# Kernel tuning notes

Hardware: AMD Instinct MI355X
Metric: run time of the kernel (lower is better)

Reference implementation:

```python
import jax, jax.numpy as jnp
import numpy as np

DIM = 384; HEADS = 16; HEAD_DIM = DIM // HEADS; HID = 4 * DIM
ETA_SCALE = 0.01; CLIP_INNER = 1.0; EPS = 1e-5
B = 8; T_FR = 32; GH = 16; GW = 16; CHUNK = 8; N = T_FR * GH * GW
D_SEG = 2 * (HEAD_DIM // 3 // 2)  # 8 dims each for t/h/w rotation (3*8 == head_dim)


def _layernorm(x, g, b):
    m = jnp.mean(x, -1, keepdims=True)
    v = jnp.var(x, -1, keepdims=True)
    return (x - m) * jax.lax.rsqrt(v + EPS) * g + b


def _mlp(W1, b1, W2, b2, x):
    # 2-layer Titan memory / CMS level MLP: dim -> 4*dim -> dim, GELU
    return jax.nn.gelu(x @ W1 + b1) @ W2 + b2


def _rope_seg(x, pos):
    # x: [..., s] interleaved-pair RoPE with positions pos (broadcastable to x[..., 0])
    s = x.shape[-1]; half = s // 2
    freqs = 1.0 / (10000.0 ** (jnp.arange(half, dtype=x.dtype) / half))
    ang = pos[..., None] * freqs
    c, si = jnp.cos(ang), jnp.sin(ang)
    x1, x2 = x[..., 0::2], x[..., 1::2]
    return jnp.stack([x1 * c - x2 * si, x1 * si + x2 * c], -1).reshape(x.shape)


def _apply_rope(x, tp, hp, wp):
    # 3D RoPE per head over (t, h, w) position segments
    b, n, d = x.shape
    xh = x.reshape(b, n, HEADS, HEAD_DIM)
    s = D_SEG
    parts = [_rope_seg(xh[..., 0:s], tp[None, :, None]),
             _rope_seg(xh[..., s:2 * s], hp[None, :, None]),
             _rope_seg(xh[..., 2 * s:3 * s], wp[None, :, None])]
    if 3 * s < HEAD_DIM:
        parts.append(xh[..., 3 * s:])
    return jnp.concatenate(parts, -1).reshape(b, n, d)


def _forward(x, norm1_g, norm1_b, q_W, tW1, tb1, tW2, tb2, out_W, out_b,
             norm2_g, norm2_b, cms_W1, cms_b1, cms_W2, cms_b2, T, H, W, chunk_size):
    Bx, Nt, D = x.shape
    y = _layernorm(x, norm1_g, norm1_b)
    nc = T // chunk_size
    Cper = chunk_size * H * W
    y_ch = y.reshape(Bx, nc, Cper, D).swapaxes(0, 1)  # [nc, B, Cper, D]
    # per-chunk RoPE positions (positions restart each chunk, matching _titan_forward_chunk)
    tp = jnp.repeat(jnp.arange(chunk_size, dtype=x.dtype), H * W)
    hp = jnp.tile(jnp.repeat(jnp.arange(H, dtype=x.dtype), W), chunk_size)
    wp = jnp.tile(jnp.arange(W, dtype=x.dtype), chunk_size * H)

    def mem_loss(W1, b1, W2, b2, kk, tt):
        return jnp.mean((_mlp(W1, b1, W2, b2, kk) - tt) ** 2)

    grad_fn = jax.grad(mem_loss, argnums=(0, 1, 2, 3))
    mlp_v = jax.vmap(_mlp, in_axes=(0, 0, 0, 0, None))

    def step(carry, yc):
        W1s, b1s, W2s, b2s = carry  # stacked [5, ...]: k, v, eta, alpha, memory
        gen = mlp_v(W1s[:4], b1s[:4], W2s[:4], b2s[:4], yc)  # [4, B, C, D]
        k, v, eta_raw, alpha_raw = gen[0], gen[1], gen[2], gen[3]
        eta = jax.nn.softplus(eta_raw) * ETA_SCALE
        alpha = jax.nn.sigmoid(alpha_raw)
        q = yc @ q_W
        q = _apply_rope(q, tp, hp, wp)
        k = _apply_rope(k, tp, hp, wp)
        out = _mlp(W1s[4], b1s[4], W2s[4], b2s[4], q)  # retrieve from main memory
        # surprise signal (per-token retrieval error norm); threshold=0 -> always update
        # surprise = jnp.linalg.norm(v - out, axis=-1)
        # self-targets v_hat = M_box(v) for the 4 adaptive memories; main memory targets v
        vhat = mlp_v(W1s[:4], b1s[:4], W2s[:4], b2s[:4], v)
        targets = jnp.concatenate([jax.lax.stop_gradient(vhat), v[None]], 0)  # [5,B,C,D]
        g1, g2, g3, g4 = jax.vmap(grad_fn, in_axes=(0, 0, 0, 0, None, 0))(
            W1s, b1s, W2s, b2s, k, targets)
        norm = jnp.sqrt(jnp.sum(g1 * g1, (1, 2)) + jnp.sum(g2 * g2, 1)
                        + jnp.sum(g3 * g3, (1, 2)) + jnp.sum(g4 * g4, 1))
        sc = jnp.minimum(1.0, CLIP_INNER / (norm + 1e-12))  # inner grad clip per memory
        em = jnp.mean(eta); am = jnp.mean(alpha)
        # DGD update with decay alpha and lr eta: p <- (1-alpha)*p - eta*g
        W1n = (1 - am) * W1s - em * g1 * sc[:, None, None]
        b1n = (1 - am) * b1s - em * g2 * sc[:, None]
        W2n = (1 - am) * W2s - em * g3 * sc[:, None, None]
        b2n = (1 - am) * b2s - em * g4 * sc[:, None]
        return (W1n, b1n, W2n, b2n), out

    _, outs = jax.lax.scan(step, (tW1, tb1, tW2, tb2), y_ch)
    titan = outs.swapaxes(0, 1).reshape(Bx, Nt, D) @ out_W + out_b
    x2 = x + titan
    # Phase B: CMS multi-frequency MLP cascade (sequential chain of level MLPs)
    h = _layernorm(x2, norm2_g, norm2_b)
    for l in range(cms_W1.shape[0]):
        h = _mlp(cms_W1[l], cms_b1[l], cms_W2[l], cms_b2[l], h)
    return x2 + h


def setup_inputs() -> dict:
    key = jax.random.key(0)
    ks = jax.random.split(key, 8)
    s = 0.02
    f = jnp.float32
    return {
        'x': jax.random.normal(ks[0], (B, N, DIM), f),
        'norm1_g': jnp.ones((DIM,), f), 'norm1_b': jnp.zeros((DIM,), f),
        'q_W': jax.random.normal(ks[1], (DIM, DIM), f) * s,
        'tW1': jax.random.normal(ks[2], (5, DIM, HID), f) * s,
        'tb1': jnp.zeros((5, HID), f),
        'tW2': jax.random.normal(ks[3], (5, HID, DIM), f) * s,
        'tb2': jnp.zeros((5, DIM), f),
        'out_W': jax.random.normal(ks[4], (DIM, DIM), f) * s,
        'out_b': jnp.zeros((DIM,), f),
        'norm2_g': jnp.ones((DIM,), f), 'norm2_b': jnp.zeros((DIM,), f),
        'cms_W1': jax.random.normal(ks[5], (3, DIM, HID), f) * s,
        'cms_b1': jnp.zeros((3, HID), f),
        'cms_W2': jax.random.normal(ks[6], (3, HID, DIM), f) * s,
        'cms_b2': jnp.zeros((3, DIM), f),
        'T': T_FR, 'H': GH, 'W': GW, 'chunk_size': CHUNK,
    }


def reference(x, norm1_g, norm1_b, q_W, tW1, tb1, tW2, tb2, out_W, out_b,
              norm2_g, norm2_b, cms_W1, cms_b1, cms_W2, cms_b2, T, H, W, chunk_size):
    return _forward(x, norm1_g, norm1_b, q_W, tW1, tb1, tW2, tb2, out_W, out_b,
                    norm2_g, norm2_b, cms_W1, cms_b1, cms_W2, cms_b2, T, H, W, chunk_size)
```

## Files before the change

### kernel.cpp

```cpp
#include <hip/hip_runtime.h>
#include <cstddef>
#include <cstdint>


typedef __bf16 bf16;
typedef __bf16 bf16x4 __attribute__((ext_vector_type(4)));
typedef __bf16 bf16x8 __attribute__((ext_vector_type(8)));
typedef float  f32x4  __attribute__((ext_vector_type(4)));

constexpr float INV_CNT = 1.0f / 6291456.0f;

__device__ __forceinline__ float fast_gelu(float x) {
  float u = 0.7978845608028654f * (x + 0.044715f * x * x * x);
  return x / (1.0f + __expf(-2.0f * u));
}
__device__ __forceinline__ f32x4 gelu4(f32x4 v) {
  v[0] = fast_gelu(v[0]); v[1] = fast_gelu(v[1]);
  v[2] = fast_gelu(v[2]); v[3] = fast_gelu(v[3]);
  return v;
}
__device__ __forceinline__ void gelu_both4(f32x4 v, f32x4& g, f32x4& gp) {
#pragma unroll
  for (int e = 0; e < 4; ++e) {
    float x = v[e];
    float x2 = x * x;
    float u = 0.7978845608028654f * (x + 0.044715f * x * x2);
    float s = 1.0f / (1.0f + __expf(-2.0f * u));
    g[e]  = x * s;
    gp[e] = s + x * s * (1.0f - s) * 1.5957691216057308f * (1.0f + 0.134145f * x2);
  }
}
__device__ __forceinline__ bf16x4 tobf4(f32x4 v) {
  bf16x4 o; o[0] = (bf16)v[0]; o[1] = (bf16)v[1]; o[2] = (bf16)v[2]; o[3] = (bf16)v[3];
  return o;
}
__device__ __forceinline__ f32x4 tof4(bf16x4 v) {
  return f32x4{(float)v[0], (float)v[1], (float)v[2], (float)v[3]};
}

__device__ __forceinline__ void gload16(const bf16* g, void* lds) {
  __builtin_amdgcn_global_load_lds(
      (const __attribute__((address_space(1))) void*)g,
      (__attribute__((address_space(3))) void*)lds, 16, 0, 0);
}

template <int N>
__device__ __forceinline__ void wait_vmcnt() {
  if constexpr (N == 0)      asm volatile("s_waitcnt vmcnt(0)" ::: "memory");
  else if constexpr (N == 2) asm volatile("s_waitcnt vmcnt(2)" ::: "memory");
  else if constexpr (N == 3) asm volatile("s_waitcnt vmcnt(3)" ::: "memory");
  else if constexpr (N == 4) asm volatile("s_waitcnt vmcnt(4)" ::: "memory");
  __builtin_amdgcn_sched_barrier(0);
}

__device__ __forceinline__ int xcd_chunk(int id, int n) {
  int q = n >> 3, r = n & 7;
  int xcd = id & 7, pos = id >> 3;
  return (xcd < r ? xcd * (q + 1) : r * (q + 1) + (xcd - r) * q) + pos;
}

__global__ __launch_bounds__(64)
void ln_kernel(const float* __restrict__ x, const float* __restrict__ g,
               const float* __restrict__ b, bf16* __restrict__ y,
               int shift, int base, int stride) {
  int r = blockIdx.x;
  int src = ((r >> shift) * stride) + base + (r & ((1 << shift) - 1));
  int lane = threadIdx.x;
  const float* xr = x + (size_t)src * 384;
  float vals[6];
  float s = 0.f, s2 = 0.f;
#pragma unroll
  for (int i = 0; i < 6; ++i) {
    float v = xr[lane + i * 64];
    vals[i] = v; s += v; s2 += v * v;
  }
#pragma unroll
  for (int o = 32; o > 0; o >>= 1) { s += __shfl_xor(s, o); s2 += __shfl_xor(s2, o); }
  float m = s * (1.0f / 384.0f);
  float var = s2 * (1.0f / 384.0f) - m * m;
  float rr = rsqrtf(var + 1e-5f);
  bf16* yr = y + (size_t)r * 384;
#pragma unroll
  for (int i = 0; i < 6; ++i) {
    int c = lane + i * 64;
    yr[c] = (bf16)((vals[i] - m) * rr * g[c] + b[c]);
  }
}

__device__ __forceinline__ void trw_body(const float* in, bf16* out, int R, int C,
                                         int c0, int r0, int tid) {
  __shared__ float t[32][33];
  int tr = tid >> 3, tc = (tid & 7) * 4;
  f32x4 v = *(const f32x4*)&in[(size_t)(r0 + tr) * C + c0 + tc];
  t[tr][tc + 0] = v[0]; t[tr][tc + 1] = v[1]; t[tr][tc + 2] = v[2]; t[tr][tc + 3] = v[3];
  __syncthreads();
  bf16x4 o;
  o[0] = (bf16)t[tc + 0][tr]; o[1] = (bf16)t[tc + 1][tr];
  o[2] = (bf16)t[tc + 2][tr]; o[3] = (bf16)t[tc + 3][tr];
  *(bf16x4*)&out[(size_t)(c0 + tr) * R + r0 + tc] = o;
}

__global__ __launch_bounds__(256)
void trans_state(const float* __restrict__ SW1, const float* __restrict__ SW2,
                 bf16* __restrict__ sw1t, bf16* __restrict__ sw2t) {
  int z = blockIdx.z;
  if (z < 5)
    trw_body(SW1 + (size_t)z * 589824, sw1t + (size_t)z * 589824, 384, 1536,
             blockIdx.x * 32, blockIdx.y * 32, threadIdx.x);
  else
    trw_body(SW2 + (size_t)(z - 5) * 589824, sw2t + (size_t)(z - 5) * 589824, 1536, 384,
             blockIdx.y * 32, blockIdx.x * 32, threadIdx.x);
}

__global__ __launch_bounds__(256)
void trans_static(const float* __restrict__ qW, const float* __restrict__ outW,
                  const float* __restrict__ cW1, const float* __restrict__ cW2,
                  bf16* __restrict__ qwt, bf16* __restrict__ owt,
                  bf16* __restrict__ cw1t, bf16* __restrict__ cw2t) {
  int z = blockIdx.z;
  if (z < 2) {
    if (blockIdx.x >= 12) return;
    trw_body(z ? outW : qW, z ? owt : qwt, 384, 384,
             blockIdx.x * 32, blockIdx.y * 32, threadIdx.x);
  } else if (z < 5) {
    int lc = z - 2;
    trw_body(cW1 + (size_t)lc * 589824, cw1t + (size_t)lc * 589824, 384, 1536,
             blockIdx.x * 32, blockIdx.y * 32, threadIdx.x);
  } else {
    int lc = z - 5;
    trw_body(cW2 + (size_t)lc * 589824, cw2t + (size_t)lc * 589824, 1536, 384,
             blockIdx.y * 32, blockIdx.x * 32, threadIdx.x);
  }
}

__global__ __launch_bounds__(256)
void tr_bf(const bf16* __restrict__ in, bf16* __restrict__ out, int R, int C) {
  __shared__ bf16 t[32][36];
  int r0 = blockIdx.x * 32, c0 = blockIdx.y * 32;
  int tr = threadIdx.x >> 3, tc = (threadIdx.x & 7) * 4;
  bf16x4 v = *(const bf16x4*)&in[(size_t)(r0 + tr) * C + c0 + tc];
  t[tr][tc + 0] = v[0]; t[tr][tc + 1] = v[1]; t[tr][tc + 2] = v[2]; t[tr][tc + 3] = v[3];
  __syncthreads();
  bf16x4 o;
  o[0] = t[tc + 0][tr]; o[1] = t[tc + 1][tr]; o[2] = t[tc + 2][tr]; o[3] = t[tc + 3][tr];
  *(bf16x4*)&out[(size_t)(c0 + tr) * R + r0 + tc] = o;
}

__global__ __launch_bounds__(256)
void copy_bf16(const float* __restrict__ in, bf16* __restrict__ out, int n) {
  int i = (blockIdx.x * 256 + threadIdx.x) * 4;
  if (i < n) {
    f32x4 v = *(const f32x4*)&in[i];
    *(bf16x4*)&out[i] = tobf4(v);
  }
}

enum { E_BF16 = 0, E_GELU, E_PAIR, E_PAIRD, E_SUB, E_SCL, E_MUL, E_F32ADD, E_KV, E_RED2 };

template <int EPI, int BM>
__global__ __launch_bounds__(BM == 128 ? 512 : 256)
void mm_fwd(const bf16* __restrict__ Act, int lda, const bf16* __restrict__ W,
            const float* __restrict__ bias, const bf16* __restrict__ baux,
            const float* __restrict__ faux, float* __restrict__ red,
            bf16* __restrict__ Cb, bf16* __restrict__ C2, bf16* __restrict__ Ct,
            float* __restrict__ Cf, int K, int ldc, int ldt, float scale,
            int croff, int cshift, int cbase, int cstride,
            long zA, long zW, int zB) {
  constexpr int NW = (BM == 128) ? 8 : 4;
  constexpr int NFM = 2;
  constexpr int TW = 8 / NW;
  constexpr int TA = (BM / 16) / NW;
  constexpr int LPT = TW + TA;
  constexpr int SWE = 128 * 32;
  constexpr int SAE = BM * 32;
  constexpr int BUFE = 2 * (SWE + SAE);
  constexpr int SLABE = NW * 16 * 68 * 2;
  constexpr int SMEME = (BUFE > SLABE) ? BUFE : SLABE;
  constexpr bool TRANS = (EPI == E_PAIR || EPI == E_PAIRD || EPI == E_SUB ||
                          EPI == E_SCL || EPI == E_MUL);
  __shared__ bf16 smem[SMEME];
  const int z = blockIdx.z;
  Act += (size_t)z * zA;
  W   += (size_t)z * zW;
  if (bias) bias += (size_t)z * zB;
  const int nx = gridDim.x;
  const int nid = xcd_chunk(blockIdx.y * nx + blockIdx.x, nx * gridDim.y);
  const int m0 = (nid / nx) * BM, i0 = (nid % nx) * 128;
  const int tid = threadIdx.x;
  const int l = tid & 63, w = tid >> 6;
  const int a = l & 15, g = l >> 4;
  const int wi0 = (w & 1) * 64, wm0 = (w >> 1) * 32;
  const int srow = l >> 2;
  const int sue = ((l & 3) ^ ((l >> 3) & 3)) * 8;
  const int fru = (g ^ ((a >> 1) & 3)) << 4;

  const bf16* wp = W   + (size_t)(i0 + srow) * K   + sue;
  const bf16* ap = Act + (size_t)(m0 + srow) * lda + sue;

  f32x4 acc[4][NFM];
#pragma unroll
  for (int i = 0; i < 4; ++i)
#pragma unroll
    for (int j = 0; j < NFM; ++j) acc[i][j] = f32x4{0.f, 0.f, 0.f, 0.f};

  auto stage = [&](int buf, int k0) {
    bf16* dW = smem + buf * SWE;
    bf16* dA = smem + 2 * SWE + buf * SAE;
#pragma unroll
    for (int t = 0; t < TW; ++t) {
      const int seg = w * TW + t;
      gload16(wp + (size_t)(seg * 16) * K + k0, (char*)dW + seg * 1024);
    }
#pragma unroll
    for (int t = 0; t < TA; ++t) {
      const int seg = w * TA + t;
      gload16(ap + (size_t)(seg * 16) * lda + k0, (char*)dA + seg * 1024);
    }
  };

  const int nIt = K >> 5;
  stage(0, 0);
  for (int it = 0; it < nIt; ++it) {
    const int cur = it & 1;
    if (it + 1 < nIt) { stage(cur ^ 1, (it + 1) << 5); wait_vmcnt<LPT>(); }
    else              { wait_vmcnt<0>(); }
    __builtin_amdgcn_s_barrier();
    const bf16* bW = smem + cur * SWE;
    const bf16* bA = smem + 2 * SWE + cur * SAE;
    {
      bf16x8 Af[4], Bf[NFM];
#pragma unroll
      for (int f = 0; f < 4; ++f) {
        const int rW = wi0 + f * 16 + a;
        Af[f] = *(const bf16x8*)((const char*)bW + rW * 64 + fru);
      }
#pragma unroll
      for (int f = 0; f < NFM; ++f) {
        const int rA = wm0 + f * 16 + a;
        Bf[f] = *(const bf16x8*)((const char*)bA + rA * 64 + fru);
      }
#pragma unroll
      for (int fi = 0; fi < 4; ++fi)
#pragma unroll
        for (int fm = 0; fm < NFM; ++fm)
          acc[fi][fm] = __builtin_amdgcn_mfma_f32_16x16x32_bf16(Af[fi], Bf[fm], acc[fi][fm], 0, 0, 0);
    }
    asm volatile("s_waitcnt lgkmcnt(0)" ::: "memory");
    __builtin_amdgcn_s_barrier();
  }

  if constexpr (EPI == E_RED2) {
    float ssum = 0.f;
#pragma unroll
    for (int fi = 0; fi < 4; ++fi) {
      f32x4 b4 = *(const f32x4*)&bias[i0 + wi0 + fi * 16 + g * 4];
#pragma unroll
      for (int fm = 0; fm < NFM; ++fm)
#pragma unroll
        for (int r = 0; r < 4; ++r) {
          float vv = acc[fi][fm][r] + b4[r];
          if (z == 0) ssum += fmaxf(vv, 0.f) + log1pf(__expf(-fabsf(vv)));
          else        ssum += 1.0f / (1.0f + __expf(-vv));
        }
    }
#pragma unroll
    for (int o = 32; o > 0; o >>= 1) ssum += __shfl_xor(ssum, o);
    float* wred = (float*)smem;
    if (l == 0) wred[w] = ssum;
    __syncthreads();
    if (tid == 0) {
      float t2 = 0.f;
      for (int q = 0; q < NW; ++q) t2 += wred[q];
      atomicAdd(&red[z], t2);
    }
    return;
  } else {
    float* T = (float*)smem + w * (16 * 68);
    const int iB = i0 + wi0;
    f32x4 b4 = f32x4{0.f, 0.f, 0.f, 0.f};
    if (bias) b4 = *(const f32x4*)&bias[iB + a * 4];
#pragma unroll
    for (int fm = 0; fm < NFM; ++fm) {
#pragma unroll
      for (int fi = 0; fi < 4; ++fi)
        *(f32x4*)&T[a * 68 + fi * 16 + g * 4] = acc[fi][fm];
      asm volatile("s_waitcnt lgkmcnt(0)" ::: "memory");
      __builtin_amdgcn_sched_barrier(0);

#pragma unroll
      for (int q = 0; q < 4; ++q) {
        const int ml = wm0 + fm * 16 + q * 4 + g;
        const int trow = q * 4 + g;
        f32x4 v = *(const f32x4*)&T[trow * 68 + a * 4];
        v += b4;
        if constexpr (EPI == E_F32ADD) {
          const int rr = croff + m0 + ml;
          const int crow = ((rr >> cshift) * cstride) + cbase + (rr & ((1 << cshift) - 1));
          const size_t cb = (size_t)crow * ldc + iB + a * 4;
          v += *(const f32x4*)&faux[cb];
          *(f32x4*)&Cf[cb] = v;
        } else {
          const size_t cb = (size_t)(m0 + ml) * ldc + iB + a * 4;
          if constexpr (EPI == E_BF16) {
            *(bf16x4*)&Cb[cb] = tobf4(v);
          } else if constexpr (EPI == E_KV) {
            bf16* DST = (z == 0) ? Cb : C2;
            *(bf16x4*)&DST[cb] = tobf4(v);
          } else if constexpr (EPI == E_GELU) {
            *(bf16x4*)&Cb[cb] = tobf4(gelu4(v));
          } else if constexpr (EPI == E_PAIR) {
            f32x4 gv, gp;
            gelu_both4(v, gv, gp);
            *(bf16x4*)&Cb[cb] = tobf4(gp);
            *(bf16x4*)&C2[cb] = tobf4(gv);
            *(f32x4*)&T[trow * 68 + a * 4] = gv;
          } else if constexpr (EPI == E_PAIRD) {
            f32x4 gv, gp;
            gelu_both4(v, gv, gp);
            f32x4 d = gv - tof4(*(const bf16x4*)&baux[cb]);
            *(bf16x4*)&Cb[cb] = tobf4(gp);
            *(bf16x4*)&C2[cb] = tobf4(d);
            *(f32x4*)&T[trow * 68 + a * 4] = gv;
          } else if constexpr (EPI == E_SUB) {
            f32x4 t4 = tof4(*(const bf16x4*)&baux[cb]);
            v = (v - t4) * scale;
            *(bf16x4*)&Cb[cb] = tobf4(v);
            *(f32x4*)&T[trow * 68 + a * 4] = v;
          } else if constexpr (EPI == E_SCL) {
            v = v * scale;
            *(bf16x4*)&Cb[cb] = tobf4(v);
            *(f32x4*)&T[trow * 68 + a * 4] = v;
          } else if constexpr (EPI == E_MUL) {
            f32x4 h4 = tof4(*(const bf16x4*)&baux[cb]);
            v *= h4;
            *(f32x4*)&T[trow * 68 + a * 4] = v;
          }
        }
      }

      if constexpr (TRANS) {
        asm volatile("s_waitcnt lgkmcnt(0)" ::: "memory");
        __builtin_amdgcn_sched_barrier(0);
        const int mg = m0 + wm0 + fm * 16;
        bf16x8 o0, o1;
#pragma unroll
        for (int j = 0; j < 16; ++j) {
          float vv = T[j * 68 + l];
          if (j < 8) o0[j] = (bf16)vv; else o1[j - 8] = (bf16)vv;
        }
        *(bf16x8*)&Ct[(size_t)(iB + l) * ldt + mg] = o0;
        *(bf16x8*)&Ct[(size_t)(iB + l) * ldt + mg + 8] = o1;
      }
    }
  }
}

__global__ __launch_bounds__(512)
void mm_tn2c(const bf16* __restrict__ P1, int ldP1, const bf16* __restrict__ Q1, int ldQ1,
             float* __restrict__ Ga, int ldGa,
             const bf16* __restrict__ P2, int ldP2, const bf16* __restrict__ Q2, int ldQ2,
             float* __restrict__ Gb, int ldGb, int mlen,
             float* __restrict__ G4s, float* __restrict__ G2s) {
  constexpr int SBE = 128 * 32;
  __shared__ bf16 smem[4 * SBE];
  const int nid = xcd_chunk(blockIdx.x, gridDim.x);
  const int grp = nid / 36, pair = nid % 36;
  const int part = grp & 1, zsl = grp >> 1;
  const bf16* P; const bf16* Q; float* G; float* Gsum;
  int ldP, ldQ, ldG, p0, q0;
  if (part == 0) {
    P = P1; Q = Q1; G = Ga; ldP = ldP1; ldQ = ldQ1; ldG = ldGa; Gsum = G4s;
    p0 = (pair / 3) * 128; q0 = (pair % 3) * 128;
  } else {
    P = P2; Q = Q2; G = Gb; ldP = ldP2; ldQ = ldQ2; ldG = ldGb; Gsum = G2s;
    p0 = (pair / 12) * 128; q0 = (pair % 12) * 128;
  }
  const bool doSum = (p0 == 0);
  const int tid = threadIdx.x;
  const int mb = zsl * mlen;
  const int l = tid & 63, w = tid >> 6;
  const int a = l & 15, g = l >> 4;
  const int wp0 = (w & 1) * 64, wq0 = (w >> 1) * 32;
  const int sue = ((l & 3) ^ ((l >> 3) & 3)) * 8;
  const int fru = (g ^ ((a >> 1) & 3)) << 4;

  const bf16* pP = P + (size_t)(p0 + w * 16 + (l >> 2)) * ldP + sue;
  const bf16* pQ = Q + (size_t)(q0 + w * 16 + (l >> 2)) * ldQ + sue;

  f32x4 acc[4][2];
#pragma unroll
  for (int i = 0; i < 4; ++i)
#pragma unroll
    for (int j = 0; j < 2; ++j) acc[i][j] = f32x4{0.f, 0.f, 0.f, 0.f};
  float qsum = 0.f;
  const int sumoff = (w * 16 + (l >> 2)) * 64 + (l & 3) * 16;

  auto stage = [&](int buf, int m0) {
    bf16* dP = smem + buf * SBE;
    bf16* dQ = smem + 2 * SBE + buf * SBE;
    gload16(pP + m0, (char*)dP + w * 1024);
    gload16(pQ + m0, (char*)dQ + w * 1024);
  };

  const int nIt = mlen >> 5;
  stage(0, mb);
  for (int it = 0; it < nIt; ++it) {
    const int cur = it & 1;
    if (it + 1 < nIt) { stage(cur ^ 1, mb + ((it + 1) << 5)); wait_vmcnt<2>(); }
    else              { wait_vmcnt<0>(); }
    __builtin_amdgcn_s_barrier();
    const bf16* bP = smem + cur * SBE;
    const bf16* bQ = smem + 2 * SBE + cur * SBE;
    {
      bf16x8 Pf[4], Qf[2];
#pragma unroll
      for (int f = 0; f < 4; ++f) {
        const int rP = wp0 + f * 16 + a;
        Pf[f] = *(const bf16x8*)((const char*)bP + rP * 64 + fru);
      }
#pragma unroll
      for (int f = 0; f < 2; ++f) {
        const int rQ = wq0 + f * 16 + a;
        Qf[f] = *(const bf16x8*)((const char*)bQ + rQ * 64 + fru);
      }
#pragma unroll
      for (int f1 = 0; f1 < 4; ++f1)
#pragma unroll
        for (int f2 = 0; f2 < 2; ++f2)
          acc[f1][f2] = __builtin_amdgcn_mfma_f32_16x16x32_bf16(Pf[f1], Qf[f2], acc[f1][f2], 0, 0, 0);
    }
    if (doSum) {
      bf16x8 s0 = *(const bf16x8*)((const char*)bQ + sumoff);
#pragma unroll
      for (int e = 0; e < 8; ++e) qsum += (float)s0[e];
    }
    asm volatile("s_waitcnt lgkmcnt(0)" ::: "memory");
    __builtin_amdgcn_s_barrier();
  }
#pragma unroll
  for (int f1 = 0; f1 < 4; ++f1)
#pragma unroll
    for (int f2 = 0; f2 < 2; ++f2)
#pragma unroll
      for (int r = 0; r < 4; ++r)
        atomicAdd(&G[(size_t)(p0 + wp0 + f1 * 16 + g * 4 + r) * ldG + q0 + wq0 + f2 * 16 + a],
                  acc[f1][f2][r]);
  if (doSum) {
    qsum += __shfl_xor(qsum, 1);
    qsum += __shfl_xor(qsum, 2);
    if ((l & 3) == 0) atomicAdd(&Gsum[q0 + w * 16 + (l >> 2)], qsum);
  }
}

__global__ __launch_bounds__(256)
void rope_kernel(bf16* __restrict__ qb, int rbase) {
  int idx = blockIdx.x * blockDim.x + threadIdx.x;
  int row = idx >> 4, hd = idx & 15;
  int j = (rbase + row) & 2047;
  float pos[3] = { (float)(j >> 8), (float)((j >> 4) & 15), (float)(j & 15) };
  const float freqs[4] = { 1.0f, 0.1f, 0.01f, 0.001f };
  bf16* p = qb + (size_t)row * 384 + hd * 24;
#pragma unroll
  for (int s = 0; s < 3; ++s) {
    bf16x8 vv = *(bf16x8*)(p + s * 8);
#pragma unroll
    for (int pr = 0; pr < 4; ++pr) {
      float ang = pos[s] * freqs[pr];
      float si, co;
      sincosf(ang, &si, &co);
      float e0 = (float)vv[2 * pr], e1 = (float)vv[2 * pr + 1];
      vv[2 * pr]     = (bf16)(e0 * co - e1 * si);
      vv[2 * pr + 1] = (bf16)(e0 * si + e1 * co);
    }
    *(bf16x8*)(p + s * 8) = vv;
  }
}

__global__ __launch_bounds__(256)
void sumsq_all(const float* __restrict__ G1, const float* __restrict__ G2,
               const float* __restrict__ G3, const float* __restrict__ G4,
               float* __restrict__ red) {
  int i = blockIdx.y, bx = blockIdx.x;
  const float* base; int per, lb, nb;
  if (bx < 256)      { base = G1 + (size_t)i * 589824; per = 589824; lb = bx;       nb = 256; }
  else if (bx < 512) { base = G3 + (size_t)i * 589824; per = 589824; lb = bx - 256; nb = 256; }
  else if (bx < 514) { base = G2 + (size_t)i * 1536;   per = 1536;   lb = bx - 512; nb = 2; }
  else               { base = G4 + (size_t)i * 384;    per = 384;    lb = bx - 514; nb = 2; }
  float s = 0.f;
  for (int idx = lb * 256 + threadIdx.x; idx < per; idx += nb * 256) {
    float v = base[idx]; s += v * v;
  }
  __shared__ float sm[256];
  sm[threadIdx.x] = s; __syncthreads();
  for (int o = 128; o > 0; o >>= 1) {
    if (threadIdx.x < o) sm[threadIdx.x] += sm[threadIdx.x + o];
    __syncthreads();
  }
  if (threadIdx.x == 0) atomicAdd(&red[2 + i], sm[0]);
}

__global__ __launch_bounds__(256)
void update_all(float* __restrict__ SW1, float* __restrict__ SB1,
                float* __restrict__ SW2, float* __restrict__ SB2,
                const float* __restrict__ G1, const float* __restrict__ G2,
                const float* __restrict__ G3, const float* __restrict__ G4,
                const float* __restrict__ red) {
  int i = blockIdx.y, bx = blockIdx.x;
  float* S; const float* G; int per, lb, nb;
  if (bx < 512)       { S = SW1; G = G1; per = 589824; lb = bx;        nb = 512; }
  else if (bx < 1024) { S = SW2; G = G3; per = 589824; lb = bx - 512;  nb = 512; }
  else if (bx < 1028) { S = SB1; G = G2; per = 1536;   lb = bx - 1024; nb = 4; }
  else                { S = SB2; G = G4; per = 384;    lb = bx - 1028; nb = 4; }
  size_t base = (size_t)i * per;
  float em = 0.01f * red[0] * INV_CNT;
  float am = red[1] * INV_CNT;
  float norm = sqrtf(red[2 + i]);
  float sc = fminf(1.0f, 1.0f / (norm + 1e-12f));
  float ws_ = 1.0f - am;
  float gs = em * sc;
  for (int idx = lb * 256 + (int)threadIdx.x; idx < per; idx += nb * 256)
    S[base + idx] = ws_ * S[base + idx] - gs * G[base + idx];
}

extern "C" void kernel_launch(void* const* d_in, const int* in_sizes, int n_in,
                              void* d_out, int out_size, void* d_ws, size_t ws_size,
                              hipStream_t stream) {
  const float* x    = (const float*)d_in[0];
  const float* n1g  = (const float*)d_in[1];
  const float* n1b  = (const float*)d_in[2];
  const float* qW   = (const float*)d_in[3];
  const float* tW1  = (const float*)d_in[4];
  const float* tb1  = (const float*)d_in[5];
  const float* tW2  = (const float*)d_in[6];
  const float* tb2  = (const float*)d_in[7];
  const float* outW = (const float*)d_in[8];
  const float* outb = (const float*)d_in[9];
  const float* n2g  = (const float*)d_in[10];
  const float* n2b  = (const float*)d_in[11];
  const float* cW1  = (const float*)d_in[12];
  const float* cb1  = (const float*)d_in[13];
  const float* cW2  = (const float*)d_in[14];
  const float* cb2  = (const float*)d_in[15];
  float* out = (float*)d_out;

  const size_t W1SZ = 384 * 1536, W2SZ = 1536 * 384;
  const size_t STATE = 5 * W1SZ + 5 * 1536 + 5 * W2SZ + 5 * 384;
  const size_t BF_W = 21 * W1SZ + 2 * 147456;
  const size_t CHUNK_BF = 4 * (size_t)16384 * 384;
  const size_t FIXEDF = 2 * STATE + 16 + BF_W / 2 + CHUNK_BF / 2;
  size_t MS = 16384;
  while (MS > 2048 && (FIXEDF + MS * 3840) * 4 > ws_size) MS >>= 1;
  if ((FIXEDF + MS * 3840) * 4 > ws_size) {
    hipMemcpyAsync(d_out, d_in[0], (size_t)25165824 * 4, hipMemcpyDeviceToDevice, stream);
    return;
  }
  const int NS = (int)(16384 / MS);
  const int iMS = (int)MS;

  float* ws = (float*)d_ws;
  size_t off = 0;
  auto alloc = [&](size_t n) { float* p = ws + off; off += n; return p; };
  auto balloc = [&](size_t n) { bf16* p = (bf16*)(ws + off); off += (n + 1) / 2; return p; };
  float* SW1 = alloc(5 * W1SZ);
  float* SB1 = alloc(5 * 1536);
  float* SW2 = alloc(5 * W2SZ);
  float* SB2 = alloc(5 * 384);
  float* G1  = alloc(5 * W1SZ);
  float* G2  = alloc(5 * 1536);
  float* G3  = alloc(5 * W2SZ);
  float* G4  = alloc(5 * 384);
  float* RED = alloc(16);
  bf16* Yc   = balloc((size_t)16384 * 384);
  bf16* Kb   = balloc((size_t)16384 * 384);
  bf16* Vb   = balloc((size_t)16384 * 384);
  bf16* Kbt  = balloc((size_t)16384 * 384);
  bf16* sw1t = balloc(5 * W1SZ);
  bf16* sw2t = balloc(5 * W2SZ);
  bf16* sw2c = balloc(5 * W2SZ);
  bf16* qwt  = balloc(147456);
  bf16* owt  = balloc(147456);
  bf16* cw1t = balloc(3 * W1SZ);
  bf16* cw2t = balloc(3 * W2SZ);
  bf16* pool = balloc(MS * 3072);
  bf16* GH1t = balloc(MS * 1536);
  bf16* DAt  = balloc(MS * 1536);
  bf16* OD   = balloc(MS * 384);
  bf16* ODt  = balloc(MS * 384);
  bf16* T2   = balloc(MS * 384);
  bf16* Tt   = balloc(MS * 384);
  bf16* H1r  = pool;
  bf16* GH1k = pool + MS * 1536;

  hipMemcpyAsync(SW1, tW1, 5 * W1SZ * 4, hipMemcpyDeviceToDevice, stream);
  hipMemcpyAsync(SB1, tb1, 5 * 1536 * 4, hipMemcpyDeviceToDevice, stream);
  hipMemcpyAsync(SW2, tW2, 5 * W2SZ * 4, hipMemcpyDeviceToDevice, stream);
  hipMemcpyAsync(SB2, tb2, 5 * 384 * 4, hipMemcpyDeviceToDevice, stream);

  trans_static<<<dim3(48, 12, 8), 256, 0, stream>>>(qW, outW, cW1, cW2, qwt, owt, cw1t, cw2t);

  const size_t grads_bytes = STATE * 4;
  const int gm  = iMS / 128;
  const int gm2 = iMS / 64;
  int mlen_t = iMS / 8; if (mlen_t < 128) mlen_t = 128;
  if (mlen_t > 2048) mlen_t = 2048;
  const int nzt = iMS / mlen_t;
  const int tn_grid = 36 * 2 * nzt;
  const float SC = 2.0f * INV_CNT;
  const size_t MSR = (size_t)iMS * 384;

  for (int c = 0; c < 4; ++c) {
    hipMemsetAsync(G1, 0, grads_bytes, stream);
    hipMemsetAsync(RED, 0, 64, stream);
    trans_state<<<dim3(48, 12, 10), 256, 0, stream>>>(SW1, SW2, sw1t, sw2t);
    copy_bf16<<<dim3(2880), 256, 0, stream>>>(SW2, sw2c, (int)(5 * W2SZ));

    ln_kernel<<<dim3(16384), dim3(64), 0, stream>>>(x, n1g, n1b, Yc, 11, c * 2048, 8192);

    for (int s = 0; s < NS; ++s) {
      const bf16* Ys = Yc + (size_t)s * MSR;
      mm_fwd<E_GELU, 128><<<dim3(24, gm), 512, 0, stream>>>(Ys, 384, sw1t,
          SB1, nullptr, nullptr, nullptr, pool, nullptr, nullptr, nullptr,
          384, 3072, 0, 0.f, 0, 30, 0, 0, 0, 0, 0);
      mm_fwd<E_KV, 64><<<dim3(3, gm2, 2), 256, 0, stream>>>(pool, 3072, sw2t,
          SB2, nullptr, nullptr, nullptr, Kb + s * MSR, Vb + s * MSR, nullptr, nullptr,
          1536, 384, 0, 0.f, 0, 30, 0, 0, 1536, (long)W2SZ, 384);
      mm_fwd<E_GELU, 128><<<dim3(24, gm), 512, 0, stream>>>(Ys, 384, sw1t + 2 * W1SZ,
          SB1 + 2 * 1536, nullptr, nullptr, nullptr, pool, nullptr, nullptr, nullptr,
          384, 3072, 0, 0.f, 0, 30, 0, 0, 0, 0, 0);
      mm_fwd<E_RED2, 64><<<dim3(3, gm2, 2), 256, 0, stream>>>(pool, 3072, sw2t + 2 * W2SZ,
          SB2 + 2 * 384, nullptr, nullptr, RED, nullptr, nullptr, nullptr, nullptr,
          1536, 384, 0, 0.f, 0, 30, 0, 0, 1536, (long)W2SZ, 384);
    }

    for (int s = 0; s < NS; ++s) {
      const bf16* Ys = Yc + (size_t)s * MSR;
      mm_fwd<E_BF16, 64><<<dim3(3, gm2), 256, 0, stream>>>(Ys, 384, qwt,
          nullptr, nullptr, nullptr, nullptr, Tt, nullptr, nullptr, nullptr,
          384, 384, 0, 0.f, 0, 30, 0, 0, 0, 0, 0);
      rope_kernel<<<dim3(iMS / 16), 256, 0, stream>>>(Tt, s * iMS);
      mm_fwd<E_GELU, 128><<<dim3(12, gm), 512, 0, stream>>>(Tt, 384, sw1t + 4 * W1SZ,
          SB1 + 4 * 1536, nullptr, nullptr, nullptr, GH1k, nullptr, nullptr, nullptr,
          384, 1536, 0, 0.f, 0, 30, 0, 0, 0, 0, 0);
      mm_fwd<E_BF16, 64><<<dim3(3, gm2), 256, 0, stream>>>(GH1k, 1536, sw2t + 4 * W2SZ,
          SB2 + 4 * 384, nullptr, nullptr, nullptr, T2, nullptr, nullptr, nullptr,
          1536, 384, 0, 0.f, 0, 30, 0, 0, 0, 0, 0);
      mm_fwd<E_F32ADD, 64><<<dim3(3, gm2), 256, 0, stream>>>(T2, 384, owt, outb,
          nullptr, x, nullptr, nullptr, nullptr, nullptr, out,
          384, 384, 0, 0.f, s * iMS, 11, c * 2048, 8192, 0, 0, 0);
    }

    rope_kernel<<<dim3(1024), 256, 0, stream>>>(Kb, 0);
    tr_bf<<<dim3(512, 12), 256, 0, stream>>>(Kb, Kbt, 16384, 384);

    for (int s = 0; s < NS; ++s) {
      const bf16* Ks = Kb + (size_t)s * MSR;
      const bf16* Vs = Vb + (size_t)s * MSR;
      for (int i = 0; i < 5; ++i) {
        if (i < 4) {
          mm_fwd<E_GELU, 128><<<dim3(12, gm), 512, 0, stream>>>(Vs, 384, sw1t + i * W1SZ,
              SB1 + i * 1536, nullptr, nullptr, nullptr, GH1k, nullptr, nullptr, nullptr,
              384, 1536, 0, 0.f, 0, 30, 0, 0, 0, 0, 0);
          mm_fwd<E_PAIRD, 128><<<dim3(12, gm), 512, 0, stream>>>(Ks, 384, sw1t + i * W1SZ,
              SB1 + i * 1536, GH1k, nullptr, nullptr, H1r, DAt, GH1t, nullptr,
              384, 1536, iMS, 0.f, 0, 30, 0, 0, 0, 0, 0);
          mm_fwd<E_SCL, 64><<<dim3(3, gm2), 256, 0, stream>>>(DAt, 1536, sw2t + i * W2SZ,
              nullptr, nullptr, nullptr, nullptr, OD, nullptr, ODt, nullptr,
              1536, 384, iMS, SC, 0, 30, 0, 0, 0, 0, 0);
        } else {
          mm_fwd<E_PAIR, 128><<<dim3(12, gm), 512, 0, stream>>>(Ks, 384, sw1t + 4 * W1SZ,
              SB1 + 4 * 1536, nullptr, nullptr, nullptr, H1r, GH1k, GH1t, nullptr,
              384, 1536, iMS, 0.f, 0, 30, 0, 0, 0, 0, 0);
          mm_fwd<E_SUB, 64><<<dim3(3, gm2), 256, 0, stream>>>(GH1k, 1536, sw2t + 4 * W2SZ,
              SB2 + 4 * 384, Vs, nullptr, nullptr, OD, nullptr, ODt, nullptr,
              1536, 384, iMS, SC, 0, 30, 0, 0, 0, 0, 0);
        }
        mm_fwd<E_MUL, 128><<<dim3(12, gm), 512, 0, stream>>>(OD, 384, sw2c + i * W2SZ,
            nullptr, H1r, nullptr, nullptr, nullptr, nullptr, DAt, nullptr,
            384, 1536, iMS, 0.f, 0, 30, 0, 0, 0, 0, 0);
        mm_tn2c<<<dim3(tn_grid), 512, 0, stream>>>(
            GH1t, iMS, ODt, iMS, G3 + i * W2SZ, 384,
            Kbt + (size_t)s * iMS, 16384, DAt, iMS, G1 + i * W1SZ, 1536, mlen_t,
            G4 + i * 384, G2 + i * 1536);
      }
    }

    sumsq_all<<<dim3(516, 5), 256, 0, stream>>>(G1, G2, G3, G4, RED);
    update_all<<<dim3(1032, 5), 256, 0, stream>>>(SW1, SB1, SW2, SB2, G1, G2, G3, G4, RED);
  }

  const int NCS = (int)(65536 / MS);
  for (int s2 = 0; s2 < NCS; ++s2) {
    float* outp = out + (size_t)s2 * MSR;
    ln_kernel<<<dim3(iMS), dim3(64), 0, stream>>>(out, n2g, n2b, OD, 30, s2 * iMS, 0);
    bf16* hc = OD; bf16* hn = T2;
    for (int lc = 0; lc < 3; ++lc) {
      mm_fwd<E_GELU, 128><<<dim3(12, gm), 512, 0, stream>>>(hc, 384, cw1t + lc * W1SZ,
          cb1 + lc * 1536, nullptr, nullptr, nullptr, GH1k, nullptr, nullptr, nullptr,
          384, 1536, 0, 0.f, 0, 30, 0, 0, 0, 0, 0);
      if (lc < 2) {
        mm_fwd<E_BF16, 64><<<dim3(3, gm2), 256, 0, stream>>>(GH1k, 1536, cw2t + lc * W2SZ,
            cb2 + lc * 384, nullptr, nullptr, nullptr, hn, nullptr, nullptr, nullptr,
            1536, 384, 0, 0.f, 0, 30, 0, 0, 0, 0, 0);
        bf16* t = hc; hc = hn; hn = t;
      } else {
        mm_fwd<E_F32ADD, 64><<<dim3(3, gm2), 256, 0, stream>>>(GH1k, 1536, cw2t + lc * W2SZ,
            cb2 + lc * 384, nullptr, outp, nullptr, nullptr, nullptr, nullptr, outp,
            1536, 384, 0, 0.f, 0, 30, 0, 0, 0, 0, 0);
      }
    }
  }
}
```

Baseline: 8.814 ms.

## Fuse V-side GELU matmul into PAIRD kernel, keeping target activations in registers

```diff
diff --git a/kernel.cpp b/kernel.cpp
--- a/kernel.cpp
+++ b/kernel.cpp
@@ -176,8 +176,7 @@
   constexpr int BUFE = 2 * (SWE + SAE);
   constexpr int SLABE = NW * 16 * 68 * 2;
   constexpr int SMEME = (BUFE > SLABE) ? BUFE : SLABE;
-  constexpr bool TRANS = (EPI == E_PAIR || EPI == E_PAIRD || EPI == E_SUB ||
-                          EPI == E_SCL || EPI == E_MUL);
+  constexpr bool TRANS = (EPI == E_PAIR || EPI == E_SUB || EPI == E_SCL || EPI == E_MUL);
   __shared__ bf16 smem[SMEME];
   const int z = blockIdx.z;
   Act += (size_t)z * zA;
@@ -203,51 +202,66 @@
 #pragma unroll
     for (int j = 0; j < NFM; ++j) acc[i][j] = f32x4{0.f, 0.f, 0.f, 0.f};
 
-  auto stage = [&](int buf, int k0) {
-    bf16* dW = smem + buf * SWE;
-    bf16* dA = smem + 2 * SWE + buf * SAE;
-#pragma unroll
-    for (int t = 0; t < TW; ++t) {
-      const int seg = w * TW + t;
-      gload16(wp + (size_t)(seg * 16) * K + k0, (char*)dW + seg * 1024);
-    }
-#pragma unroll
-    for (int t = 0; t < TA; ++t) {
-      const int seg = w * TA + t;
-      gload16(ap + (size_t)(seg * 16) * lda + k0, (char*)dA + seg * 1024);
+  auto run_loop = [&](const bf16* ab) {
+    auto stg = [&](int buf, int k0) {
+      bf16* dW = smem + buf * SWE;
+      bf16* dA = smem + 2 * SWE + buf * SAE;
+#pragma unroll
+      for (int t = 0; t < TW; ++t) {
+        const int seg = w * TW + t;
+        gload16(wp + (size_t)(seg * 16) * K + k0, (char*)dW + seg * 1024);
+      }
+#pragma unroll
+      for (int t = 0; t < TA; ++t) {
+        const int seg = w * TA + t;
+        gload16(ab + (size_t)(seg * 16) * lda + k0, (char*)dA + seg * 1024);
+      }
+    };
+    const int nIt = K >> 5;
+    stg(0, 0);
+    for (int it = 0; it < nIt; ++it) {
+      const int cur = it & 1;
+      if (it + 1 < nIt) { stg(cur ^ 1, (it + 1) << 5); wait_vmcnt<LPT>(); }
+      else              { wait_vmcnt<0>(); }
+      __builtin_amdgcn_s_barrier();
+      const bf16* bW = smem + cur * SWE;
+      const bf16* bA = smem + 2 * SWE + cur * SAE;
+      {
+        bf16x8 Af[4], Bf[NFM];
+#pragma unroll
+        for (int f = 0; f < 4; ++f) {
+          const int rW = wi0 + f * 16 + a;
+          Af[f] = *(const bf16x8*)((const char*)bW + rW * 64 + fru);
+        }
+#pragma unroll
+        for (int f = 0; f < NFM; ++f) {
+          const int rA = wm0 + f * 16 + a;
+          Bf[f] = *(const bf16x8*)((const char*)bA + rA * 64 + fru);
+        }
+#pragma unroll
+        for (int fi = 0; fi < 4; ++fi)
+#pragma unroll
+          for (int fm = 0; fm < NFM; ++fm)
+            acc[fi][fm] = __builtin_amdgcn_mfma_f32_16x16x32_bf16(Af[fi], Bf[fm], acc[fi][fm], 0, 0, 0);
+      }
+      asm volatile("s_waitcnt lgkmcnt(0)" ::: "memory");
+      __builtin_amdgcn_s_barrier();
     }
   };
 
-  const int nIt = K >> 5;
-  stage(0, 0);
-  for (int it = 0; it < nIt; ++it) {
-    const int cur = it & 1;
-    if (it + 1 < nIt) { stage(cur ^ 1, (it + 1) << 5); wait_vmcnt<LPT>(); }
-    else              { wait_vmcnt<0>(); }
-    __builtin_amdgcn_s_barrier();
-    const bf16* bW = smem + cur * SWE;
-    const bf16* bA = smem + 2 * SWE + cur * SAE;
-    {
-      bf16x8 Af[4], Bf[NFM];
-#pragma unroll
-      for (int f = 0; f < 4; ++f) {
-        const int rW = wi0 + f * 16 + a;
-        Af[f] = *(const bf16x8*)((const char*)bW + rW * 64 + fru);
-      }
-#pragma unroll
-      for (int f = 0; f < NFM; ++f) {
-        const int rA = wm0 + f * 16 + a;
-        Bf[f] = *(const bf16x8*)((const char*)bA + rA * 64 + fru);
-      }
-#pragma unroll
-      for (int fi = 0; fi < 4; ++fi)
-#pragma unroll
-        for (int fm = 0; fm < NFM; ++fm)
-          acc[fi][fm] = __builtin_amdgcn_mfma_f32_16x16x32_bf16(Af[fi], Bf[fm], acc[fi][fm], 0, 0, 0);
-    }
-    asm volatile("s_waitcnt lgkmcnt(0)" ::: "memory");
-    __builtin_amdgcn_s_barrier();
-  }
+  bf16x4 ghv[4][NFM];
+  if constexpr (EPI == E_PAIRD) {
+    run_loop(baux + (size_t)(m0 + srow) * lda + sue);
+#pragma unroll
+    for (int fi = 0; fi < 4; ++fi)
+#pragma unroll
+      for (int fm = 0; fm < NFM; ++fm) {
+        f32x4 bb = *(const f32x4*)&bias[i0 + wi0 + fi * 16 + g * 4];
+        ghv[fi][fm] = tobf4(gelu4(acc[fi][fm] + bb));
+        acc[fi][fm] = f32x4{0.f, 0.f, 0.f, 0.f};
+      }
+  }
+  run_loop(ap);
 
   if constexpr (EPI == E_RED2) {
     float ssum = 0.f;
@@ -281,6 +295,62 @@
     if (bias) b4 = *(const f32x4*)&bias[iB + a * 4];
 #pragma unroll
     for (int fm = 0; fm < NFM; ++fm) {
+      if constexpr (EPI == E_PAIRD) {
+        f32x4 gvk[4], gpk[4], ddk[4];
+#pragma unroll
+        for (int fi = 0; fi < 4; ++fi) {
+          f32x4 bb = *(const f32x4*)&bias[iB + fi * 16 + g * 4];
+          f32x4 vv = acc[fi][fm] + bb;
+          f32x4 gv, gp;
+          gelu_both4(vv, gv, gp);
+          gvk[fi] = gv; gpk[fi] = gp;
+          ddk[fi] = gv - tof4(ghv[fi][fm]);
+        }
+#pragma unroll
+        for (int fi = 0; fi < 4; ++fi)
+          *(f32x4*)&T[a * 68 + fi * 16 + g * 4] = gpk[fi];
+        asm volatile("s_waitcnt lgkmcnt(0)" ::: "memory");
+        __builtin_amdgcn_sched_barrier(0);
+#pragma unroll
+        for (int q = 0; q < 4; ++q) {
+          const int ml = wm0 + fm * 16 + q * 4 + g;
+          const size_t cb = (size_t)(m0 + ml) * ldc + iB + a * 4;
+          *(bf16x4*)&Cb[cb] = tobf4(*(const f32x4*)&T[(q * 4 + g) * 68 + a * 4]);
+        }
+        asm volatile("s_waitcnt lgkmcnt(0)" ::: "memory");
+        __builtin_amdgcn_sched_barrier(0);
+#pragma unroll
+        for (int fi = 0; fi < 4; ++fi)
+          *(f32x4*)&T[a * 68 + fi * 16 + g * 4] = ddk[fi];
+        asm volatile("s_waitcnt lgkmcnt(0)" ::: "memory");
+        __builtin_amdgcn_sched_barrier(0);
+#pragma unroll
+        for (int q = 0; q < 4; ++q) {
+          const int ml = wm0 + fm * 16 + q * 4 + g;
+          const size_t cb = (size_t)(m0 + ml) * ldc + iB + a * 4;
+          *(bf16x4*)&C2[cb] = tobf4(*(const f32x4*)&T[(q * 4 + g) * 68 + a * 4]);
+        }
+        asm volatile("s_waitcnt lgkmcnt(0)" ::: "memory");
+        __builtin_amdgcn_sched_barrier(0);
+#pragma unroll
+        for (int fi = 0; fi < 4; ++fi)
+          *(f32x4*)&T[a * 68 + fi * 16 + g * 4] = gvk[fi];
+        asm volatile("s_waitcnt lgkmcnt(0)" ::: "memory");
+        __builtin_amdgcn_sched_barrier(0);
+        {
+          const int mg = m0 + wm0 + fm * 16;
+          bf16x8 o0, o1;
+#pragma unroll
+          for (int j = 0; j < 16; ++j) {
+            float vv = T[j * 68 + l];
+            if (j < 8) o0[j] = (bf16)vv; else o1[j - 8] = (bf16)vv;
+          }
+          *(bf16x8*)&Ct[(size_t)(iB + l) * ldt + mg] = o0;
+          *(bf16x8*)&Ct[(size_t)(iB + l) * ldt + mg + 8] = o1;
+        }
+        continue;
+      }
+
 #pragma unroll
       for (int fi = 0; fi < 4; ++fi)
         *(f32x4*)&T[a * 68 + fi * 16 + g * 4] = acc[fi][fm];
@@ -313,13 +383,6 @@
             gelu_both4(v, gv, gp);
             *(bf16x4*)&Cb[cb] = tobf4(gp);
             *(bf16x4*)&C2[cb] = tobf4(gv);
-            *(f32x4*)&T[trow * 68 + a * 4] = gv;
-          } else if constexpr (EPI == E_PAIRD) {
-            f32x4 gv, gp;
-            gelu_both4(v, gv, gp);
-            f32x4 d = gv - tof4(*(const bf16x4*)&baux[cb]);
-            *(bf16x4*)&Cb[cb] = tobf4(gp);
-            *(bf16x4*)&C2[cb] = tobf4(d);
             *(f32x4*)&T[trow * 68 + a * 4] = gv;
           } else if constexpr (EPI == E_SUB) {
             f32x4 t4 = tof4(*(const bf16x4*)&baux[cb]);
@@ -657,11 +720,8 @@
       const bf16* Vs = Vb + (size_t)s * MSR;
       for (int i = 0; i < 5; ++i) {
         if (i < 4) {
-          mm_fwd<E_GELU, 128><<<dim3(12, gm), 512, 0, stream>>>(Vs, 384, sw1t + i * W1SZ,
-              SB1 + i * 1536, nullptr, nullptr, nullptr, GH1k, nullptr, nullptr, nullptr,
-              384, 1536, 0, 0.f, 0, 30, 0, 0, 0, 0, 0);
           mm_fwd<E_PAIRD, 128><<<dim3(12, gm), 512, 0, stream>>>(Ks, 384, sw1t + i * W1SZ,
-              SB1 + i * 1536, GH1k, nullptr, nullptr, H1r, DAt, GH1t, nullptr,
+              SB1 + i * 1536, Vs, nullptr, nullptr, H1r, DAt, GH1t, nullptr,
               384, 1536, iMS, 0.f, 0, 30, 0, 0, 0, 0, 0);
           mm_fwd<E_SCL, 64><<<dim3(3, gm2), 256, 0, stream>>>(DAt, 1536, sw2t + i * W2SZ,
               nullptr, nullptr, nullptr, nullptr, OD, nullptr, ODt, nullptr,
```

After: 8.362 ms. 1.05x faster.
